# Optimization experiments

Measured on AMD Instinct MI355X. Metric: run time of the kernel, lower is better.

Reference implementation:

```python
import jax, jax.numpy as jnp
import numpy as np

D = 128
NODE_COUNTS = (200000, 3000, 20000)  # operation, machine, job
E = 500000
EDGE_TYPES = [(s, t) for s in range(3) for t in range(3)]  # itertools.product order
BN_EPS = 1e-5


def setup_inputs() -> dict:
    key = jax.random.key(0)
    ks = jax.random.split(key, 40)
    x_operation = jax.random.normal(ks[0], (NODE_COUNTS[0], D), dtype=jnp.float32)
    x_machine = jax.random.normal(ks[1], (NODE_COUNTS[1], D), dtype=jnp.float32)
    x_job = jax.random.normal(ks[2], (NODE_COUNTS[2], D), dtype=jnp.float32)
    # edge_index[k] = [src_idx, dst_idx] for edge type k=(s,t)
    eis = []
    for k, (s, t) in enumerate(EDGE_TYPES):
        src = jax.random.randint(ks[3 + 2 * k], (E,), 0, NODE_COUNTS[s], dtype=jnp.int32)
        dst = jax.random.randint(ks[4 + 2 * k], (E,), 0, NODE_COUNTS[t], dtype=jnp.int32)
        eis.append(jnp.stack([src, dst]))
    edge_index = jnp.stack(eis)  # [9, 2, E]
    scale = 1.0 / np.sqrt(D)
    W1 = jax.random.normal(ks[30], (3, D, D), dtype=jnp.float32) * scale
    b1 = jnp.zeros((3, D), dtype=jnp.float32)
    g1 = jnp.ones((3, D), dtype=jnp.float32)
    be1 = jnp.zeros((3, D), dtype=jnp.float32)
    W2 = jax.random.normal(ks[31], (3, D, D), dtype=jnp.float32) * scale
    b2 = jnp.zeros((3, D), dtype=jnp.float32)
    g2 = jnp.ones((3, D), dtype=jnp.float32)
    be2 = jnp.zeros((3, D), dtype=jnp.float32)
    eps = jnp.zeros((9,), dtype=jnp.float32)  # GINConv train_eps init 0 per edge type
    return {"x_operation": x_operation, "x_machine": x_machine, "x_job": x_job,
            "edge_index": edge_index, "W1": W1, "b1": b1, "g1": g1, "be1": be1,
            "W2": W2, "b2": b2, "g2": g2, "be2": be2, "eps": eps}


def _bn(h, gamma, beta):
    # BatchNorm1d in training mode: batch stats, biased variance
    mean = h.mean(axis=0)
    var = h.var(axis=0)
    return (h - mean) * jax.lax.rsqrt(var + BN_EPS) * gamma + beta


def reference(x_operation, x_machine, x_job, edge_index, W1, b1, g1, be1, W2, b2, g2, be2, eps):
    xs = [x_operation, x_machine, x_job]

    def mlp(h, i):
        h = jax.nn.relu(_bn(h @ W1[i] + b1[i], g1[i], be1[i]))
        h = jax.nn.relu(_bn(h @ W2[i] + b2[i], g2[i], be2[i]))
        return h

    outs = [jnp.zeros((n, D), dtype=jnp.float32) for n in NODE_COUNTS]
    for k, (s, t) in enumerate(EDGE_TYPES):
        src, dst = edge_index[k, 0], edge_index[k, 1]
        # gather source features along edges, scatter-add into destinations
        agg = jax.ops.segment_sum(xs[s][src], dst, num_segments=NODE_COUNTS[t])
        h = mlp((1.0 + eps[k]) * xs[t] + agg, s)  # GINConv: nn keyed by SOURCE type
        outs[t] = outs[t] + h  # HeteroConv aggr='sum' per destination type
    return jnp.concatenate(outs, axis=0)  # [sum(NODE_COUNTS), D]
```

## Files before the change

kernel.cpp:

```cpp
#include <hip/hip_runtime.h>
#include <hip/hip_fp16.h>

#define D 128
#define E_PER 500000
#define TOT_ROWS 669000
#define CH 4096
#define NR64 64
#define SLABSZ ((size_t)223000 * 256)

typedef _Float16 f16;
typedef _Float16 f16x8 __attribute__((ext_vector_type(8)));
typedef _Float16 f16x4 __attribute__((ext_vector_type(4)));
typedef _Float16 f16x2 __attribute__((ext_vector_type(2)));
typedef float f32x4 __attribute__((ext_vector_type(4)));

__device__ const int d_SEGB[9] = {0, 200000, 203000, 223000, 423000, 426000,
                                  446000, 646000, 649000};
__device__ const int d_XB[3] = {0, 200000, 203000};
__device__ const int d_NC[3] = {200000, 3000, 20000};
__device__ const int d_T64LO[3] = {0, 3125, 3172};
__device__ const int d_T64HI[3] = {3125, 3172, 3485};

__device__ __forceinline__ unsigned a_swz(int row, int byteoff) {
    return (unsigned)(row * 256 + byteoff) ^ (unsigned)((row & 7) << 4);
}

__device__ __forceinline__ void tile_map64(int g, int& t, int& tl) {
    if (g < 3125)      { t = 0; tl = g; }
    else if (g < 3172) { t = 1; tl = g - 3125; }
    else               { t = 2; tl = g - 3172; }
}

__global__ void precast(const float* __restrict__ W1,
                        const float* __restrict__ W2,
                        f16* __restrict__ Wth) {
    int i = blockIdx.x * 256 + threadIdx.x;
    if (i >= 2 * 3 * 128 * 128) return;
    int layer = i / 49152;
    int rem = i - layer * 49152;
    int s = rem / 16384;
    int r2 = rem & 16383;
    int kk = r2 >> 7;
    int c  = r2 & 127;
    const float* W = layer ? W2 : W1;
    Wth[(((size_t)layer * 3 + s) * 128 + c) * 128 + kk] = (f16)W[((size_t)s * 128 + kk) * 128 + c];
}

__global__ void cast16_all(const float* __restrict__ x0,
                           const float* __restrict__ x1,
                           const float* __restrict__ x2,
                           f16* __restrict__ y) {
    const int total = 223000 * 16;
    for (int i = blockIdx.x * 256 + threadIdx.x; i < total; i += gridDim.x * 256) {
        int row = i >> 4, c8 = i & 15;
        const float* src;
        if (row < 200000)      src = x0 + (size_t)row * D;
        else if (row < 203000) src = x1 + (size_t)(row - 200000) * D;
        else                   src = x2 + (size_t)(row - 203000) * D;
        f32x4 v0 = ((const f32x4*)src)[c8 * 2];
        f32x4 v1 = ((const f32x4*)src)[c8 * 2 + 1];
        f16x8 h;
        #pragma unroll
        for (int j = 0; j < 4; ++j) { h[j] = (f16)v0[j]; h[4 + j] = (f16)v1[j]; }
        ((f16x8*)(y + (size_t)row * D))[c8] = h;
    }
}

__global__ __launch_bounds__(256) void bucket_count(const int* __restrict__ ei,
                                                    int* __restrict__ bcnt) {
    __shared__ int hist[256];
    int k = blockIdx.y, tid = threadIdx.x;
    const int* dstp = ei + (size_t)k * 2 * E_PER + E_PER;
    unsigned Nt = (unsigned)d_NC[k % 3];
    int base = blockIdx.x * CH;
    int hi = min(base + CH, E_PER);
    hist[tid] = 0;
    __syncthreads();
    for (int i = base + tid; i < hi; i += 256) {
        unsigned b = ((unsigned)dstp[i] << 8) / Nt;
        atomicAdd(&hist[b], 1);
    }
    __syncthreads();
    if (hist[tid]) atomicAdd(&bcnt[k * 256 + tid], hist[tid]);
}

__global__ void bucket_scan(const int* __restrict__ bcnt,
                            int* __restrict__ bbase, int* __restrict__ bcursor) {
    __shared__ int sb[256];
    int t = threadIdx.x;
    int loc[9];
    int s = 0;
    #pragma unroll
    for (int j = 0; j < 9; ++j) { loc[j] = bcnt[t * 9 + j]; s += loc[j]; }
    sb[t] = s; __syncthreads();
    int v = s;
    for (int off = 1; off < 256; off <<= 1) {
        int u = (t >= off) ? sb[t - off] : 0;
        __syncthreads();
        sb[t] += u;
        __syncthreads();
    }
    int pre = sb[t] - v;
    #pragma unroll
    for (int j = 0; j < 9; ++j) {
        bbase[t * 9 + j] = pre;
        bcursor[t * 9 + j] = pre;
        pre += loc[j];
    }
    if (t == 255) bbase[2304] = pre;
}

__global__ __launch_bounds__(256) void bin_scatter(const int* __restrict__ ei,
                                                   int* __restrict__ bcursor,
                                                   int2* __restrict__ binned) {
    __shared__ int hist[256], gb[256], cur[256];
    int k = blockIdx.y, tid = threadIdx.x;
    const int* srcp = ei + (size_t)k * 2 * E_PER;
    const int* dstp = srcp + E_PER;
    unsigned Nt = (unsigned)d_NC[k % 3];
    int base = blockIdx.x * CH;
    int hi = min(base + CH, E_PER);
    hist[tid] = 0;
    __syncthreads();
    for (int i = base + tid; i < hi; i += 256) {
        unsigned b = ((unsigned)dstp[i] << 8) / Nt;
        atomicAdd(&hist[b], 1);
    }
    __syncthreads();
    gb[tid] = hist[tid] ? atomicAdd(&bcursor[k * 256 + tid], hist[tid]) : 0;
    cur[tid] = 0;
    __syncthreads();
    for (int i = base + tid; i < hi; i += 256) {
        int src = srcp[i], dst = dstp[i];
        unsigned b = ((unsigned)dst << 8) / Nt;
        int r = atomicAdd(&cur[b], 1);
        binned[(size_t)gb[b] + r] = make_int2(src, dst);
    }
}

__global__ __launch_bounds__(256) void fine_fill(const int2* __restrict__ binned,
                                                 const int* __restrict__ bbase,
                                                 int* __restrict__ rowstart,
                                                 int* __restrict__ ssrc) {
    __shared__ int rcnt[784];
    __shared__ int excl[784];
    __shared__ int scur[784];
    __shared__ int sb[256];
    int k = blockIdx.y, b = blockIdx.x, tid = threadIdx.x;
    int Nt = d_NC[k % 3];
    int segb = d_SEGB[k];
    int row_lo = (b * Nt + 255) >> 8;
    int row_hi = ((b + 1) * Nt + 255) >> 8;
    int nrows = row_hi - row_lo;
    int ebase = bbase[k * 256 + b];
    int eend  = bbase[k * 256 + b + 1];
    for (int i = tid; i < nrows; i += 256) rcnt[i] = 0;
    __syncthreads();
    for (int e = ebase + tid; e < eend; e += 256)
        atomicAdd(&rcnt[binned[e].y - row_lo], 1);
    __syncthreads();
    int stride = (nrows + 255) >> 8;
    int lo = tid * stride;
    int hi2 = min(lo + stride, nrows);
    int s = 0;
    for (int i = lo; i < hi2; ++i) s += rcnt[i];
    sb[tid] = s; __syncthreads();
    int v = s;
    for (int off = 1; off < 256; off <<= 1) {
        int u = (tid >= off) ? sb[tid - off] : 0;
        __syncthreads();
        sb[tid] += u;
        __syncthreads();
    }
    int pre = sb[tid] - v;
    for (int i = lo; i < hi2; ++i) {
        excl[i] = pre;
        scur[i] = pre;
        pre += rcnt[i];
    }
    __syncthreads();
    for (int i = tid; i < nrows; i += 256)
        rowstart[segb + row_lo + i] = ebase + excl[i];
    if (k == 8 && b == 255 && tid == 0) rowstart[TOT_ROWS] = eend;
    for (int e = ebase + tid; e < eend; e += 256) {
        int2 ed = binned[e];
        int r = atomicAdd(&scur[ed.y - row_lo], 1);
        ssrc[ebase + r] = ed.x;
    }
}

__global__ __launch_bounds__(256) void aggregate_t1(const f16* __restrict__ x16,
                                                    const int* __restrict__ rowstart,
                                                    const int* __restrict__ ssrc,
                                                    char* __restrict__ slabs,
                                                    const float* __restrict__ eps9) {
    __shared__ float part[4][128];
    int row = blockIdx.x;
    int s = blockIdx.y;
    int k = s * 3 + 1;
    const int* rs = rowstart + d_SEGB[k];
    const f16* xsrc = x16 + (size_t)d_XB[s] * D;
    const f16* xt   = x16 + (size_t)d_XB[1] * D;
    char* slab = slabs + (size_t)s * SLABSZ + (size_t)d_XB[1] * 256;
    float epsv = 1.0f + eps9[k];
    int tid  = threadIdx.x;
    int lane = tid & 63;
    int w    = tid >> 6;
    int grp  = lane >> 4;
    int cs   = lane & 15;
    int estart = w * 4 + grp, estep = 16;
    float acc[8];
    #pragma unroll
    for (int j = 0; j < 8; ++j) acc[j] = 0.f;
    int e1 = rs[row + 1];
    int e  = rs[row] + estart;
    for (; e + 3 * estep < e1; e += 4 * estep) {
        int s0 = ssrc[e], s1 = ssrc[e + estep], s2 = ssrc[e + 2 * estep], s3 = ssrc[e + 3 * estep];
        f16x8 v0 = ((const f16x8*)(xsrc + (size_t)s0 * D))[cs];
        f16x8 v1 = ((const f16x8*)(xsrc + (size_t)s1 * D))[cs];
        f16x8 v2 = ((const f16x8*)(xsrc + (size_t)s2 * D))[cs];
        f16x8 v3 = ((const f16x8*)(xsrc + (size_t)s3 * D))[cs];
        #pragma unroll
        for (int j = 0; j < 8; ++j)
            acc[j] += ((float)v0[j] + (float)v1[j]) + ((float)v2[j] + (float)v3[j]);
    }
    for (; e < e1; e += estep) {
        int s0 = ssrc[e];
        f16x8 v0 = ((const f16x8*)(xsrc + (size_t)s0 * D))[cs];
        #pragma unroll
        for (int j = 0; j < 8; ++j) acc[j] += (float)v0[j];
    }
    #pragma unroll
    for (int j = 0; j < 8; ++j) {
        acc[j] += __shfl_xor(acc[j], 16);
        acc[j] += __shfl_xor(acc[j], 32);
    }
    if (lane < 16) {
        #pragma unroll
        for (int j = 0; j < 8; ++j) part[w][cs * 8 + j] = acc[j];
    }
    __syncthreads();
    if (w == 0 && lane < 16) {
        f16x8 xv = ((const f16x8*)(xt + (size_t)row * D))[cs];
        f16x8 h;
        #pragma unroll
        for (int j = 0; j < 8; ++j) {
            float v = (part[0][cs*8+j] + part[1][cs*8+j]) + (part[2][cs*8+j] + part[3][cs*8+j]);
            h[j] = (f16)(v + epsv * (float)xv[j]);
        }
        ((f16x8*)(slab + (size_t)row * 256))[cs] = h;
    }
}

__global__ __launch_bounds__(256) void gemm_l1f(char* __restrict__ slabs,
                                                const f16* __restrict__ x16,
                                                const int* __restrict__ rowstart,
                                                const int* __restrict__ ssrc,
                                                const f16* __restrict__ Wth,
                                                const float* __restrict__ b1,
                                                const float* __restrict__ eps9,
                                                float* __restrict__ partials) {
    __shared__ alignas(16) char atile[64 * 256];
    __shared__ float wst[4][256];
    const int tid  = threadIdx.x;
    const int lane = tid & 63;
    const int w    = tid >> 6;
    const int s    = blockIdx.y;
    int t, tl;
    tile_map64(blockIdx.x, t, tl);
    const int N = d_NC[t];
    const int row0 = tl * 64;
    const int k = s * 3 + t;
    char* slab = slabs + (size_t)s * SLABSZ + (size_t)d_XB[t] * 256;

    if (t != 1) {
        const f16* xsrc = x16 + (size_t)d_XB[s] * D;
        const f16* xt   = x16 + (size_t)d_XB[t] * D;
        const int* rs = rowstart + d_SEGB[k];
        const float epsv = 1.0f + eps9[k];
        const int g4 = lane >> 4;
        const int cs = lane & 15;
        const int nrows_t = min(64, N - row0);

        for (int i = 0; i < 4; ++i) {
            int r = (w << 4) + i * 4 + g4;
            int row = row0 + r;
            f16x8 h = {0, 0, 0, 0, 0, 0, 0, 0};
            if (r < nrows_t) {
                int e  = rs[row];
                int e1 = rs[row + 1];
                f16x8 xv = ((const f16x8*)(xt + (size_t)row * D))[cs];
                float acc[8];
                #pragma unroll
                for (int j = 0; j < 8; ++j) acc[j] = epsv * (float)xv[j];
                for (; e + 3 < e1; e += 4) {
                    int s0 = ssrc[e], s1 = ssrc[e + 1], s2 = ssrc[e + 2], s3 = ssrc[e + 3];
                    f16x8 v0 = ((const f16x8*)(xsrc + (size_t)s0 * D))[cs];
                    f16x8 v1 = ((const f16x8*)(xsrc + (size_t)s1 * D))[cs];
                    f16x8 v2 = ((const f16x8*)(xsrc + (size_t)s2 * D))[cs];
                    f16x8 v3 = ((const f16x8*)(xsrc + (size_t)s3 * D))[cs];
                    #pragma unroll
                    for (int j = 0; j < 8; ++j)
                        acc[j] += ((float)v0[j] + (float)v1[j]) + ((float)v2[j] + (float)v3[j]);
                }
                if (e + 1 < e1) {
                    int s0 = ssrc[e], s1 = ssrc[e + 1];
                    f16x8 v0 = ((const f16x8*)(xsrc + (size_t)s0 * D))[cs];
                    f16x8 v1 = ((const f16x8*)(xsrc + (size_t)s1 * D))[cs];
                    #pragma unroll
                    for (int j = 0; j < 8; ++j) acc[j] += (float)v0[j] + (float)v1[j];
                    e += 2;
                }
                if (e < e1) {
                    int s0 = ssrc[e];
                    f16x8 v0 = ((const f16x8*)(xsrc + (size_t)s0 * D))[cs];
                    #pragma unroll
                    for (int j = 0; j < 8; ++j) acc[j] += (float)v0[j];
                }
                #pragma unroll
                for (int j = 0; j < 8; ++j) h[j] = (f16)acc[j];
            }
            *(f16x8*)(atile + a_swz(r, cs * 16)) = h;
        }
    } else {
        #pragma unroll
        for (int p = 0; p < 4; ++p) {
            int r  = (w << 4) + p * 4 + (lane >> 4);
            int c8 = lane & 15;
            int row = row0 + r;
            if (row >= N) row = N - 1;
            const char* src = slab + (size_t)row * 256 + (unsigned)((c8 * 16) ^ ((r & 7) << 4));
            __builtin_amdgcn_global_load_lds(
                (const __attribute__((address_space(1))) void*)src,
                (__attribute__((address_space(3))) void*)(atile + w * 4096 + p * 1024),
                16, 0, 0);
        }
        __syncthreads();
    }

    const f16* Wt = Wth + (size_t)s * 16384;
    f32x4 acc0[8];
    #pragma unroll
    for (int ct = 0; ct < 8; ++ct) acc0[ct] = (f32x4){0.f, 0.f, 0.f, 0.f};
    const int arow = (w << 4) + (lane & 15);
    const int kq = (lane >> 4) * 8;
    #pragma unroll
    for (int ks = 0; ks < 4; ++ks) {
        f16x8 af = *(const f16x8*)(atile + a_swz(arow, (ks * 32 + kq) * 2));
        #pragma unroll
        for (int ct = 0; ct < 8; ++ct) {
            f16x8 bf = *(const f16x8*)(Wt + (size_t)(ct * 16 + (lane & 15)) * D + ks * 32 + kq);
            acc0[ct] = __builtin_amdgcn_mfma_f32_16x16x32_f16(af, bf, acc0[ct], 0, 0, 0);
        }
    }

    const int col_lo = lane & 15;
    const int lrb0 = (w << 4) + ((lane >> 4) << 2);
    #pragma unroll
    for (int ct = 0; ct < 8; ++ct) {
        int col = ct * 16 + col_lo;
        float bv = b1[s * D + col];
        float s_ = 0.f, q_ = 0.f;
        #pragma unroll
        for (int r = 0; r < 4; ++r) {
            int lrow = lrb0 + r;
            float val = acc0[ct][r] + bv;
            if (row0 + lrow < N) { s_ += val; q_ += val * val; }
            *(f16*)(atile + a_swz(lrow, col * 2)) = (f16)val;
        }
        s_ += __shfl_xor(s_, 16); q_ += __shfl_xor(q_, 16);
        s_ += __shfl_xor(s_, 32); q_ += __shfl_xor(q_, 32);
        if (lane < 16) { wst[w][col] = s_; wst[w][128 + col] = q_; }
    }
    __syncthreads();

    #pragma unroll
    for (int p = 0; p < 4; ++p) {
        int r  = p * 16 + (tid >> 4);
        int c8 = tid & 15;
        int row = row0 + r;
        if (row < N)
            *(f16x8*)(slab + (size_t)row * 256 + c8 * 16) = *(const f16x8*)(atile + a_swz(r, c8 * 16));
    }
    float pv = wst[0][tid] + wst[1][tid] + wst[2][tid] + wst[3][tid];
    partials[((size_t)blockIdx.x * 3 + s) * 256 + tid] = pv;
}

__global__ __launch_bounds__(256) void gemm_l2(char* __restrict__ slabs,
                                               const f16* __restrict__ Wth2,
                                               const float* __restrict__ bias,
                                               const float* __restrict__ affa,
                                               const float* __restrict__ affc,
                                               float* __restrict__ partials) {
    __shared__ alignas(16) char atile[64 * 256];
    __shared__ float wst[4][256];
    const int tid  = threadIdx.x;
    const int lane = tid & 63;
    const int w    = tid >> 6;
    const int s    = blockIdx.y;
    int t, tl;
    tile_map64(blockIdx.x, t, tl);
    const int N = d_NC[t];
    const int row0 = tl * 64;
    const int k = s * 3 + t;
    char* slab = slabs + (size_t)s * SLABSZ + (size_t)d_XB[t] * 256;
    const int c8 = lane & 15;
    const int g4 = lane >> 4;

    f32x4 a0 = ((const f32x4*)(affa + k * 128))[c8 * 2];
    f32x4 a1 = ((const f32x4*)(affa + k * 128))[c8 * 2 + 1];
    f32x4 c0 = ((const f32x4*)(affc + k * 128))[c8 * 2];
    f32x4 c1 = ((const f32x4*)(affc + k * 128))[c8 * 2 + 1];

    f16x8 zv[4];
    #pragma unroll
    for (int p = 0; p < 4; ++p) {
        int r = (w << 4) + p * 4 + g4;
        int row = row0 + r;
        zv[p] = (row < N) ? ((const f16x8*)(slab + (size_t)row * 256))[c8]
                          : (f16x8){0, 0, 0, 0, 0, 0, 0, 0};
    }
    #pragma unroll
    for (int p = 0; p < 4; ++p) {
        int r = (w << 4) + p * 4 + g4;
        f16x8 hv;
        #pragma unroll
        for (int j = 0; j < 4; ++j) {
            float t0 = (float)zv[p][j] * a0[j] + c0[j];
            float t1 = (float)zv[p][4 + j] * a1[j] + c1[j];
            hv[j]     = (f16)(t0 > 0.f ? t0 : 0.f);
            hv[4 + j] = (f16)(t1 > 0.f ? t1 : 0.f);
        }
        *(f16x8*)(atile + a_swz(r, c8 * 16)) = hv;
    }

    const f16* Wt = Wth2 + (size_t)s * 16384;
    f32x4 acc0[8];
    #pragma unroll
    for (int ct = 0; ct < 8; ++ct) acc0[ct] = (f32x4){0.f, 0.f, 0.f, 0.f};
    const int arow = (w << 4) + (lane & 15);
    const int kq = (lane >> 4) * 8;
    #pragma unroll
    for (int ks = 0; ks < 4; ++ks) {
        f16x8 af = *(const f16x8*)(atile + a_swz(arow, (ks * 32 + kq) * 2));
        #pragma unroll
        for (int ct = 0; ct < 8; ++ct) {
            f16x8 bf = *(const f16x8*)(Wt + (size_t)(ct * 16 + (lane & 15)) * D + ks * 32 + kq);
            acc0[ct] = __builtin_amdgcn_mfma_f32_16x16x32_f16(af, bf, acc0[ct], 0, 0, 0);
        }
    }

    const int col_lo = lane & 15;
    const int lrb0 = (w << 4) + ((lane >> 4) << 2);
    #pragma unroll
    for (int ct = 0; ct < 8; ++ct) {
        int col = ct * 16 + col_lo;
        float bv = bias[s * D + col];
        float s_ = 0.f, q_ = 0.f;
        #pragma unroll
        for (int r = 0; r < 4; ++r) {
            int lrow = lrb0 + r;
            float val = acc0[ct][r] + bv;
            if (row0 + lrow < N) { s_ += val; q_ += val * val; }
            *(f16*)(atile + a_swz(lrow, col * 2)) = (f16)val;
        }
        s_ += __shfl_xor(s_, 16); q_ += __shfl_xor(q_, 16);
        s_ += __shfl_xor(s_, 32); q_ += __shfl_xor(q_, 32);
        if (lane < 16) { wst[w][col] = s_; wst[w][128 + col] = q_; }
    }
    __syncthreads();

    #pragma unroll
    for (int p = 0; p < 4; ++p) {
        int r = p * 16 + (tid >> 4);
        int row = row0 + r;
        if (row < N)
            *(f16x8*)(slab + (size_t)row * 256 + (tid & 15) * 16) = *(const f16x8*)(atile + a_swz(r, (tid & 15) * 16));
    }
    float pv = wst[0][tid] + wst[1][tid] + wst[2][tid] + wst[3][tid];
    partials[((size_t)blockIdx.x * 3 + s) * 256 + tid] = pv;
}

__global__ void bn_reduce(const float* __restrict__ partials,
                          float* __restrict__ partial2) {
    int k = blockIdx.y, tid = threadIdx.x;
    int s = k / 3, t = k % 3;
    int lo = d_T64LO[t], hi = d_T64HI[t];
    float v = 0.f;
    for (int b = lo + blockIdx.x; b < hi; b += NR64)
        v += partials[((size_t)b * 3 + s) * 256 + tid];
    partial2[((size_t)k * NR64 + blockIdx.x) * 256 + tid] = v;
}

__global__ void bn_params(const float* __restrict__ partial2,
                          const float* __restrict__ g, const float* __restrict__ be,
                          float* __restrict__ affa, float* __restrict__ affc) {
    __shared__ float red[256];
    int k = blockIdx.x, tid = threadIdx.x;
    int s = k / 3, t = k % 3;
    float v = 0.f;
    #pragma unroll 4
    for (int b = 0; b < NR64; ++b)
        v += partial2[((size_t)k * NR64 + b) * 256 + tid];
    red[tid] = v;
    __syncthreads();
    if (tid < 128) {
        float sm = red[tid], q = red[128 + tid];
        float n = (float)d_NC[t];
        float mean = sm / n;
        float var  = q / n - mean * mean;
        float a = g[s * D + tid] * rsqrtf(var + 1e-5f);
        affa[k * 128 + tid] = a;
        affc[k * 128 + tid] = be[s * D + tid] - mean * a;
    }
}

__global__ __launch_bounds__(256) void accum_all(const char* __restrict__ slabs,
                                                 const float* __restrict__ affa,
                                                 const float* __restrict__ affc,
                                                 float* __restrict__ outp) {
    const int total = 223000 * 16;
    for (int i = blockIdx.x * 256 + threadIdx.x; i < total; i += gridDim.x * 256) {
        int row = i >> 4;
        int c8  = i & 15;
        int t = (row < 200000) ? 0 : (row < 203000) ? 1 : 2;
        f32x4 o0 = {0.f, 0.f, 0.f, 0.f}, o1 = {0.f, 0.f, 0.f, 0.f};
        #pragma unroll
        for (int s = 0; s < 3; ++s) {
            int k = s * 3 + t;
            f16x8 z = ((const f16x8*)(slabs + (size_t)s * SLABSZ + (size_t)row * 256))[c8];
            f32x4 a0 = ((const f32x4*)(affa + k * 128))[c8 * 2];
            f32x4 a1 = ((const f32x4*)(affa + k * 128))[c8 * 2 + 1];
            f32x4 c0 = ((const f32x4*)(affc + k * 128))[c8 * 2];
            f32x4 c1 = ((const f32x4*)(affc + k * 128))[c8 * 2 + 1];
            #pragma unroll
            for (int j = 0; j < 4; ++j) {
                float t0 = (float)z[j] * a0[j] + c0[j];
                float t1 = (float)z[4 + j] * a1[j] + c1[j];
                o0[j] += t0 > 0.f ? t0 : 0.f;
                o1[j] += t1 > 0.f ? t1 : 0.f;
            }
        }
        ((f32x4*)(outp + (size_t)row * D))[c8 * 2]     = o0;
        ((f32x4*)(outp + (size_t)row * D))[c8 * 2 + 1] = o1;
    }
}

extern "C" void kernel_launch(void* const* d_in, const int* in_sizes, int n_in,
                              void* d_out, int out_size, void* d_ws, size_t ws_size,
                              hipStream_t stream) {
    const float* x0  = (const float*)d_in[0];
    const float* x1  = (const float*)d_in[1];
    const float* x2  = (const float*)d_in[2];
    const int*   ei  = (const int*)d_in[3];
    const float* W1  = (const float*)d_in[4];
    const float* b1  = (const float*)d_in[5];
    const float* g1  = (const float*)d_in[6];
    const float* be1 = (const float*)d_in[7];
    const float* W2  = (const float*)d_in[8];
    const float* b2  = (const float*)d_in[9];
    const float* g2  = (const float*)d_in[10];
    const float* be2 = (const float*)d_in[11];
    const float* eps9 = (const float*)d_in[12];
    float* outp = (float*)d_out;

    char* ws = (char*)d_ws;
    size_t off = 0;
    char* slabs = ws;                 off += 3 * SLABSZ;
    int2* binned = (int2*)slabs;
    f16* x16    = (f16*)(ws + off);   off += SLABSZ;
    int* ssrc   = (int*)(ws + off);   off += (size_t)9 * E_PER * 4;
    int* rowstart = (int*)(ws + off); off += (size_t)(TOT_ROWS + 2) * 4;
    off = (off + 255) & ~(size_t)255;
    int* bcnt   = (int*)(ws + off);   off += 2308 * 4;
    int* bbase  = (int*)(ws + off);   off += 2308 * 4;
    int* bcursor= (int*)(ws + off);   off += 2308 * 4;
    off = (off + 255) & ~(size_t)255;
    float* partials = (float*)(ws + off); off += (size_t)3485 * 3 * 256 * 4;
    float* partial2 = (float*)(ws + off); off += (size_t)9 * NR64 * 256 * 4;
    float* aff1a = (float*)(ws + off); off += 9 * 128 * 4;
    float* aff1c = (float*)(ws + off); off += 9 * 128 * 4;
    float* aff2a = (float*)(ws + off); off += 9 * 128 * 4;
    float* aff2c = (float*)(ws + off); off += 9 * 128 * 4;
    f16* Wth = (f16*)(ws + off); off += (size_t)2 * 3 * 128 * 128 * sizeof(f16);

    precast<<<384, 256, 0, stream>>>(W1, W2, Wth);
    cast16_all<<<2048, 256, 0, stream>>>(x0, x1, x2, x16);

    hipMemsetAsync(bcnt, 0, 2308 * 4, stream);
    int nchunk = (E_PER + CH - 1) / CH;
    bucket_count<<<dim3(nchunk, 9), 256, 0, stream>>>(ei, bcnt);
    bucket_scan<<<1, 256, 0, stream>>>(bcnt, bbase, bcursor);
    bin_scatter<<<dim3(nchunk, 9), 256, 0, stream>>>(ei, bcursor, binned);
    fine_fill<<<dim3(256, 9), 256, 0, stream>>>(binned, bbase, rowstart, ssrc);

    aggregate_t1<<<dim3(3000, 3), 256, 0, stream>>>(x16, rowstart, ssrc, slabs, eps9);

    gemm_l1f<<<dim3(3485, 3), 256, 0, stream>>>(slabs, x16, rowstart, ssrc,
                                                Wth, b1, eps9, partials);
    bn_reduce<<<dim3(NR64, 9), 256, 0, stream>>>(partials, partial2);
    bn_params<<<9, 256, 0, stream>>>(partial2, g1, be1, aff1a, aff1c);

    gemm_l2<<<dim3(3485, 3), 256, 0, stream>>>(slabs, Wth + 3 * 16384, b2,
                                               aff1a, aff1c, partials);
    bn_reduce<<<dim3(NR64, 9), 256, 0, stream>>>(partials, partial2);
    bn_params<<<9, 256, 0, stream>>>(partial2, g2, be2, aff2a, aff2c);

    accum_all<<<4096, 256, 0, stream>>>(slabs, aff2a, aff2c, outp);
}
```

Measured before the change: 792.8 us.

## Split fused aggregation out of layer-1 GEMM into standalone aggregate kernel

Result: no change. 780.6 us (-1.5%).

```diff
diff --git a/kernel.cpp b/kernel.cpp
--- a/kernel.cpp
+++ b/kernel.cpp
@@ -20,6 +20,8 @@
 __device__ const int d_NC[3] = {200000, 3000, 20000};
 __device__ const int d_T64LO[3] = {0, 3125, 3172};
 __device__ const int d_T64HI[3] = {3125, 3172, 3485};
+__device__ const int d_AOFF[10] = {0, 12500, 15500, 16750, 29250, 32250,
+                                   33500, 46000, 49000, 50250};
 
 __device__ __forceinline__ unsigned a_swz(int row, int byteoff) {
     return (unsigned)(row * 256 + byteoff) ^ (unsigned)((row & 7) << 4);
@@ -189,77 +191,118 @@
     }
 }
 
-__global__ __launch_bounds__(256) void aggregate_t1(const f16* __restrict__ x16,
-                                                    const int* __restrict__ rowstart,
-                                                    const int* __restrict__ ssrc,
-                                                    char* __restrict__ slabs,
-                                                    const float* __restrict__ eps9) {
+__global__ __launch_bounds__(256) void aggregate_all(const f16* __restrict__ x16,
+                                                     const int* __restrict__ rowstart,
+                                                     const int* __restrict__ ssrc,
+                                                     char* __restrict__ slabs,
+                                                     const float* __restrict__ eps9) {
     __shared__ float part[4][128];
-    int row = blockIdx.x;
-    int s = blockIdx.y;
-    int k = s * 3 + 1;
+    int g = blockIdx.x;
+    int k = 0;
+    #pragma unroll
+    for (int j = 1; j < 9; ++j) if (g >= d_AOFF[j]) k = j;
+    int b = g - d_AOFF[k];
+    int s = k / 3, t = k % 3;
+    int N = d_NC[t];
     const int* rs = rowstart + d_SEGB[k];
     const f16* xsrc = x16 + (size_t)d_XB[s] * D;
-    const f16* xt   = x16 + (size_t)d_XB[1] * D;
-    char* slab = slabs + (size_t)s * SLABSZ + (size_t)d_XB[1] * 256;
+    const f16* xt   = x16 + (size_t)d_XB[t] * D;
+    char* slab = slabs + (size_t)s * SLABSZ + (size_t)d_XB[t] * 256;
     float epsv = 1.0f + eps9[k];
     int tid  = threadIdx.x;
     int lane = tid & 63;
     int w    = tid >> 6;
     int grp  = lane >> 4;
     int cs   = lane & 15;
-    int estart = w * 4 + grp, estep = 16;
-    float acc[8];
-    #pragma unroll
-    for (int j = 0; j < 8; ++j) acc[j] = 0.f;
-    int e1 = rs[row + 1];
-    int e  = rs[row] + estart;
-    for (; e + 3 * estep < e1; e += 4 * estep) {
-        int s0 = ssrc[e], s1 = ssrc[e + estep], s2 = ssrc[e + 2 * estep], s3 = ssrc[e + 3 * estep];
-        f16x8 v0 = ((const f16x8*)(xsrc + (size_t)s0 * D))[cs];
-        f16x8 v1 = ((const f16x8*)(xsrc + (size_t)s1 * D))[cs];
-        f16x8 v2 = ((const f16x8*)(xsrc + (size_t)s2 * D))[cs];
-        f16x8 v3 = ((const f16x8*)(xsrc + (size_t)s3 * D))[cs];
-        #pragma unroll
-        for (int j = 0; j < 8; ++j)
-            acc[j] += ((float)v0[j] + (float)v1[j]) + ((float)v2[j] + (float)v3[j]);
-    }
-    for (; e < e1; e += estep) {
-        int s0 = ssrc[e];
-        f16x8 v0 = ((const f16x8*)(xsrc + (size_t)s0 * D))[cs];
-        #pragma unroll
-        for (int j = 0; j < 8; ++j) acc[j] += (float)v0[j];
-    }
-    #pragma unroll
-    for (int j = 0; j < 8; ++j) {
-        acc[j] += __shfl_xor(acc[j], 16);
-        acc[j] += __shfl_xor(acc[j], 32);
-    }
-    if (lane < 16) {
-        #pragma unroll
-        for (int j = 0; j < 8; ++j) part[w][cs * 8 + j] = acc[j];
-    }
-    __syncthreads();
-    if (w == 0 && lane < 16) {
+
+    if (t != 1) {
+        int row = (b << 4) + (tid >> 4);
+        if (row >= N) return;
+        int e0 = rs[row], e1 = rs[row + 1];
         f16x8 xv = ((const f16x8*)(xt + (size_t)row * D))[cs];
+        float acc[8];
+        #pragma unroll
+        for (int j = 0; j < 8; ++j) acc[j] = epsv * (float)xv[j];
+        int e = e0;
+        for (; e + 3 < e1; e += 4) {
+            int s0 = ssrc[e], s1 = ssrc[e + 1], s2 = ssrc[e + 2], s3 = ssrc[e + 3];
+            f16x8 v0 = ((const f16x8*)(xsrc + (size_t)s0 * D))[cs];
+            f16x8 v1 = ((const f16x8*)(xsrc + (size_t)s1 * D))[cs];
+            f16x8 v2 = ((const f16x8*)(xsrc + (size_t)s2 * D))[cs];
+            f16x8 v3 = ((const f16x8*)(xsrc + (size_t)s3 * D))[cs];
+            #pragma unroll
+            for (int j = 0; j < 8; ++j)
+                acc[j] += ((float)v0[j] + (float)v1[j]) + ((float)v2[j] + (float)v3[j]);
+        }
+        if (e + 1 < e1) {
+            int s0 = ssrc[e], s1 = ssrc[e + 1];
+            f16x8 v0 = ((const f16x8*)(xsrc + (size_t)s0 * D))[cs];
+            f16x8 v1 = ((const f16x8*)(xsrc + (size_t)s1 * D))[cs];
+            #pragma unroll
+            for (int j = 0; j < 8; ++j) acc[j] += (float)v0[j] + (float)v1[j];
+            e += 2;
+        }
+        if (e < e1) {
+            int s0 = ssrc[e];
+            f16x8 v0 = ((const f16x8*)(xsrc + (size_t)s0 * D))[cs];
+            #pragma unroll
+            for (int j = 0; j < 8; ++j) acc[j] += (float)v0[j];
+        }
         f16x8 h;
         #pragma unroll
+        for (int j = 0; j < 8; ++j) h[j] = (f16)acc[j];
+        ((f16x8*)(slab + (size_t)row * 256))[cs] = h;
+    } else {
+        int row = b;
+        int estart = w * 4 + grp, estep = 16;
+        float acc[8];
+        #pragma unroll
+        for (int j = 0; j < 8; ++j) acc[j] = 0.f;
+        int e1 = rs[row + 1];
+        int e  = rs[row] + estart;
+        for (; e + 3 * estep < e1; e += 4 * estep) {
+            int s0 = ssrc[e], s1 = ssrc[e + estep], s2 = ssrc[e + 2 * estep], s3 = ssrc[e + 3 * estep];
+            f16x8 v0 = ((const f16x8*)(xsrc + (size_t)s0 * D))[cs];
+            f16x8 v1 = ((const f16x8*)(xsrc + (size_t)s1 * D))[cs];
+            f16x8 v2 = ((const f16x8*)(xsrc + (size_t)s2 * D))[cs];
+            f16x8 v3 = ((const f16x8*)(xsrc + (size_t)s3 * D))[cs];
+            #pragma unroll
+            for (int j = 0; j < 8; ++j)
+                acc[j] += ((float)v0[j] + (float)v1[j]) + ((float)v2[j] + (float)v3[j]);
+        }
+        for (; e < e1; e += estep) {
+            int s0 = ssrc[e];
+            f16x8 v0 = ((const f16x8*)(xsrc + (size_t)s0 * D))[cs];
+            #pragma unroll
+            for (int j = 0; j < 8; ++j) acc[j] += (float)v0[j];
+        }
+        #pragma unroll
         for (int j = 0; j < 8; ++j) {
-            float v = (part[0][cs*8+j] + part[1][cs*8+j]) + (part[2][cs*8+j] + part[3][cs*8+j]);
-            h[j] = (f16)(v + epsv * (float)xv[j]);
-        }
-        ((f16x8*)(slab + (size_t)row * 256))[cs] = h;
-    }
-}
-
-__global__ __launch_bounds__(256) void gemm_l1f(char* __restrict__ slabs,
-                                                const f16* __restrict__ x16,
-                                                const int* __restrict__ rowstart,
-                                                const int* __restrict__ ssrc,
-                                                const f16* __restrict__ Wth,
-                                                const float* __restrict__ b1,
-                                                const float* __restrict__ eps9,
-                                                float* __restrict__ partials) {
+            acc[j] += __shfl_xor(acc[j], 16);
+            acc[j] += __shfl_xor(acc[j], 32);
+        }
+        if (lane < 16) {
+            #pragma unroll
+            for (int j = 0; j < 8; ++j) part[w][cs * 8 + j] = acc[j];
+        }
+        __syncthreads();
+        if (w == 0 && lane < 16) {
+            f16x8 xv = ((const f16x8*)(xt + (size_t)row * D))[cs];
+            f16x8 h;
+            #pragma unroll
+            for (int j = 0; j < 8; ++j) {
+                float v = (part[0][cs*8+j] + part[1][cs*8+j]) + (part[2][cs*8+j] + part[3][cs*8+j]);
+                h[j] = (f16)(v + epsv * (float)xv[j]);
+            }
+            ((f16x8*)(slab + (size_t)row * 256))[cs] = h;
+        }
+    }
+}
+
+__global__ __launch_bounds__(256) void gemm_l1(char* __restrict__ slabs,
+                                               const f16* __restrict__ Wth,
+                                               const float* __restrict__ bias,
+                                               float* __restrict__ partials) {
     __shared__ alignas(16) char atile[64 * 256];
     __shared__ float wst[4][256];
     const int tid  = threadIdx.x;
@@ -270,73 +313,21 @@
     tile_map64(blockIdx.x, t, tl);
     const int N = d_NC[t];
     const int row0 = tl * 64;
-    const int k = s * 3 + t;
     char* slab = slabs + (size_t)s * SLABSZ + (size_t)d_XB[t] * 256;
 
-    if (t != 1) {
-        const f16* xsrc = x16 + (size_t)d_XB[s] * D;
-        const f16* xt   = x16 + (size_t)d_XB[t] * D;
-        const int* rs = rowstart + d_SEGB[k];
-        const float epsv = 1.0f + eps9[k];
-        const int g4 = lane >> 4;
-        const int cs = lane & 15;
-        const int nrows_t = min(64, N - row0);
-
-        for (int i = 0; i < 4; ++i) {
-            int r = (w << 4) + i * 4 + g4;
-            int row = row0 + r;
-            f16x8 h = {0, 0, 0, 0, 0, 0, 0, 0};
-            if (r < nrows_t) {
-                int e  = rs[row];
-                int e1 = rs[row + 1];
-                f16x8 xv = ((const f16x8*)(xt + (size_t)row * D))[cs];
-                float acc[8];
-                #pragma unroll
-                for (int j = 0; j < 8; ++j) acc[j] = epsv * (float)xv[j];
-                for (; e + 3 < e1; e += 4) {
-                    int s0 = ssrc[e], s1 = ssrc[e + 1], s2 = ssrc[e + 2], s3 = ssrc[e + 3];
-                    f16x8 v0 = ((const f16x8*)(xsrc + (size_t)s0 * D))[cs];
-                    f16x8 v1 = ((const f16x8*)(xsrc + (size_t)s1 * D))[cs];
-                    f16x8 v2 = ((const f16x8*)(xsrc + (size_t)s2 * D))[cs];
-                    f16x8 v3 = ((const f16x8*)(xsrc + (size_t)s3 * D))[cs];
-                    #pragma unroll
-                    for (int j = 0; j < 8; ++j)
-                        acc[j] += ((float)v0[j] + (float)v1[j]) + ((float)v2[j] + (float)v3[j]);
-                }
-                if (e + 1 < e1) {
-                    int s0 = ssrc[e], s1 = ssrc[e + 1];
-                    f16x8 v0 = ((const f16x8*)(xsrc + (size_t)s0 * D))[cs];
-                    f16x8 v1 = ((const f16x8*)(xsrc + (size_t)s1 * D))[cs];
-                    #pragma unroll
-                    for (int j = 0; j < 8; ++j) acc[j] += (float)v0[j] + (float)v1[j];
-                    e += 2;
-                }
-                if (e < e1) {
-                    int s0 = ssrc[e];
-                    f16x8 v0 = ((const f16x8*)(xsrc + (size_t)s0 * D))[cs];
-                    #pragma unroll
-                    for (int j = 0; j < 8; ++j) acc[j] += (float)v0[j];
-                }
-                #pragma unroll
-                for (int j = 0; j < 8; ++j) h[j] = (f16)acc[j];
-            }
-            *(f16x8*)(atile + a_swz(r, cs * 16)) = h;
-        }
-    } else {
-        #pragma unroll
-        for (int p = 0; p < 4; ++p) {
-            int r  = (w << 4) + p * 4 + (lane >> 4);
-            int c8 = lane & 15;
-            int row = row0 + r;
-            if (row >= N) row = N - 1;
-            const char* src = slab + (size_t)row * 256 + (unsigned)((c8 * 16) ^ ((r & 7) << 4));
-            __builtin_amdgcn_global_load_lds(
-                (const __attribute__((address_space(1))) void*)src,
-                (__attribute__((address_space(3))) void*)(atile + w * 4096 + p * 1024),
-                16, 0, 0);
-        }
-        __syncthreads();
-    }
+    #pragma unroll
+    for (int p = 0; p < 4; ++p) {
+        int r  = p * 16 + (tid >> 4);
+        int c8 = tid & 15;
+        int row = row0 + r;
+        if (row >= N) row = N - 1;
+        const char* src = slab + (size_t)row * 256 + (unsigned)((c8 * 16) ^ ((r & 7) << 4));
+        __builtin_amdgcn_global_load_lds(
+            (const __attribute__((address_space(1))) void*)src,
+            (__attribute__((address_space(3))) void*)(atile + p * 4096 + w * 1024),
+            16, 0, 0);
+    }
+    __syncthreads();
 
     const f16* Wt = Wth + (size_t)s * 16384;
     f32x4 acc0[8];
@@ -359,7 +350,7 @@
     #pragma unroll
     for (int ct = 0; ct < 8; ++ct) {
         int col = ct * 16 + col_lo;
-        float bv = b1[s * D + col];
+        float bv = bias[s * D + col];
         float s_ = 0.f, q_ = 0.f;
         #pragma unroll
         for (int r = 0; r < 4; ++r) {
@@ -594,10 +585,9 @@
     bin_scatter<<<dim3(nchunk, 9), 256, 0, stream>>>(ei, bcursor, binned);
     fine_fill<<<dim3(256, 9), 256, 0, stream>>>(binned, bbase, rowstart, ssrc);
 
-    aggregate_t1<<<dim3(3000, 3), 256, 0, stream>>>(x16, rowstart, ssrc, slabs, eps9);
-
-    gemm_l1f<<<dim3(3485, 3), 256, 0, stream>>>(slabs, x16, rowstart, ssrc,
-                                                Wth, b1, eps9, partials);
+    aggregate_all<<<50250, 256, 0, stream>>>(x16, rowstart, ssrc, slabs, eps9);
+
+    gemm_l1<<<dim3(3485, 3), 256, 0, stream>>>(slabs, Wth, b1, partials);
     bn_reduce<<<dim3(NR64, 9), 256, 0, stream>>>(partials, partial2);
     bn_params<<<9, 256, 0, stream>>>(partial2, g1, be1, aff1a, aff1c);
 
```
